# Performance work log

Hardware: AMD Instinct MI355X
Metric: run time of the kernel (lower is better)

The kernel has to match this reference:

```python
import jax, jax.numpy as jnp
import numpy as np
import math

H, KV, D, HID, WIN = 8, 4, 256, 2048, 1024  # heads, kv heads, head_dim, hidden, sliding window
B, S = 1, 2048

def _rms(x, scale):
    # Gemma3RMSNorm: hardcoded 1e-6 eps, (1+scale) gain
    var = jnp.mean(jnp.square(x), axis=-1, keepdims=True)
    return x * jax.lax.rsqrt(var + 1e-6) * (1.0 + scale)

def _rot_half(x):
    x1, x2 = jnp.split(x, 2, axis=-1)
    return jnp.concatenate((-x2, x1), axis=-1)

def setup_inputs() -> dict:
    key = jax.random.key(0)
    ks = jax.random.split(key, 8)
    x = jax.random.normal(ks[0], (B, S, HID), jnp.float32)
    attn_mask = jnp.ones((B, S), jnp.bool_)
    segment_pos = jnp.broadcast_to(jnp.arange(S, dtype=jnp.int32)[None], (B, S))
    # true RoPE tables, theta=1e6 (Gemma3 global layers)
    inv_freq = 1.0 / (1e6 ** (np.arange(0, D, 2, dtype=np.float32) / D))
    ang = np.arange(S, dtype=np.float32)[:, None] * inv_freq[None, :]  # [S, D/2]
    emb = np.concatenate([ang, ang], axis=-1)                          # [S, D]
    cos = jnp.asarray(np.cos(emb), jnp.float32)[None]                  # [1, S, D]
    sin = jnp.asarray(np.sin(emb), jnp.float32)[None]
    sd = 1.0 / math.sqrt(HID)
    wq = jax.random.normal(ks[1], (HID, H * D), jnp.float32) * sd
    wk = jax.random.normal(ks[2], (HID, KV * D), jnp.float32) * sd
    wv = jax.random.normal(ks[3], (HID, KV * D), jnp.float32) * sd
    wo = jax.random.normal(ks[4], (H * D, HID), jnp.float32) * (1.0 / math.sqrt(H * D))
    q_scale = jnp.zeros((D,), jnp.float32)  # zeros_init as in module
    k_scale = jnp.zeros((D,), jnp.float32)
    return dict(x=x, attn_mask=attn_mask, segment_pos=segment_pos, cos=cos, sin=sin,
                wq=wq, wk=wk, wv=wv, wo=wo, q_scale=q_scale, k_scale=k_scale)

def reference(x, attn_mask, segment_pos, cos, sin, wq, wk, wv, wo, q_scale, k_scale):
    b, s, _ = x.shape
    # projections -> [b, h, s, d]
    q = (x @ wq).reshape(b, s, H, D).transpose(0, 2, 1, 3)
    k = (x @ wk).reshape(b, s, KV, D).transpose(0, 2, 1, 3)
    v = (x @ wv).reshape(b, s, KV, D).transpose(0, 2, 1, 3)
    # per-head QK RMSNorm
    q = _rms(q, q_scale)
    k = _rms(k, k_scale)
    # RoPE (cos/sin broadcast over head axis, unsqueeze_dim=1)
    c, sn = cos[:, None], sin[:, None]
    q = q * c + _rot_half(q) * sn
    k = k * c + _rot_half(k) * sn
    # GQA: repeat-interleave kv heads
    rep = H // KV
    k = jnp.repeat(k, rep, axis=1)
    v = jnp.repeat(v, rep, axis=1)
    scores = jnp.einsum('bhqd,bhkd->bhqk', q, k) / math.sqrt(D)
    # causal + padding mask (q_len > 1 path, no image bidirectional mask)
    causal = jnp.tril(jnp.ones((s, s), jnp.bool_))
    mask = causal[None] & attn_mask[:, None, :]          # [b, q, kv]
    # sliding window mask (prefill: cache positions = arange)
    kvpos = jnp.arange(s)
    pos = segment_pos[:, :, None]
    sliding = (kvpos[None, None] > pos - WIN) & (kvpos[None, None] < pos + WIN)
    full = mask & sliding
    scores = scores + jnp.where(full[:, None], 0.0, -1e37)
    w = jax.nn.softmax(scores.astype(jnp.float32), axis=-1).astype(scores.dtype)
    out = jnp.einsum('bhqk,bhkd->bhqd', w, v)
    out = out.transpose(0, 2, 1, 3).reshape(b, s, H * D)
    return out @ wo
```

## Files before the change

kernel.cpp:

```cpp
#include <hip/hip_runtime.h>
#include <hip/hip_bf16.h>

#define S_LEN 2048
#define HID 2048
#define NH 8
#define NKV 4
#define HD 256
#define WIN 1024

typedef __hip_bfloat16 bf16;
typedef __attribute__((ext_vector_type(8))) short bf16x8;
typedef __attribute__((ext_vector_type(4))) float f32x4;

__device__ __forceinline__ void gld_lds16(void* lds, const void* g) {
    __builtin_amdgcn_global_load_lds(
        (const __attribute__((address_space(1))) unsigned int*)g,
        (__attribute__((address_space(3))) unsigned int*)lds,
        16, 0, 0);
}


__global__ __launch_bounds__(256)
void conv_f32_bf16(const float* __restrict__ s, bf16* __restrict__ d, int n8) {
    const int i = blockIdx.x * 256 + threadIdx.x;
    if (i >= n8) return;
    float4 a = ((const float4*)s)[i * 2];
    float4 b = ((const float4*)s)[i * 2 + 1];
    union { uint4 v; bf16 h[8]; } u;
    u.h[0] = __float2bfloat16(a.x); u.h[1] = __float2bfloat16(a.y);
    u.h[2] = __float2bfloat16(a.z); u.h[3] = __float2bfloat16(a.w);
    u.h[4] = __float2bfloat16(b.x); u.h[5] = __float2bfloat16(b.y);
    u.h[6] = __float2bfloat16(b.z); u.h[7] = __float2bfloat16(b.w);
    ((uint4*)d)[i] = u.v;
}

__device__ __forceinline__ void transT_body(const float* __restrict__ src, bf16* __restrict__ dst,
                                            int R, int C, int r0, int c0) {
    __shared__ bf16 Ts[64][72];
    const int tid = threadIdx.x;
    {
        const int r = tid >> 2;
        const int cq = (tid & 3) * 16;
#pragma unroll
        for (int j = 0; j < 16; j += 4) {
            float4 v = *(const float4*)&src[(size_t)(r0 + r) * C + c0 + cq + j];
            Ts[cq + j + 0][r] = __float2bfloat16(v.x);
            Ts[cq + j + 1][r] = __float2bfloat16(v.y);
            Ts[cq + j + 2][r] = __float2bfloat16(v.z);
            Ts[cq + j + 3][r] = __float2bfloat16(v.w);
        }
    }
    __syncthreads();
    {
        const int c = tid >> 2;
        const int rq = (tid & 3) * 16;
#pragma unroll
        for (int j = 0; j < 16; j += 8)
            *(uint4*)&dst[(size_t)(c0 + c) * R + r0 + rq + j] = *(const uint4*)&Ts[c][rq + j];
    }
}

__global__ __launch_bounds__(256)
void convT_f32_bf16(const float* __restrict__ src, bf16* __restrict__ dst, int R, int C) {
    transT_body(src, dst, R, C, blockIdx.y * 64, blockIdx.x * 64);
}

__global__ __launch_bounds__(256)
void convT_qkv(const float* __restrict__ wq, const float* __restrict__ wk,
               const float* __restrict__ wv, bf16* __restrict__ dst) {
    const int bx = blockIdx.x;
    const float* src; int C, c0, drow0;
    if (bx < 32)      { src = wq; C = 2048; c0 = bx * 64;        drow0 = bx * 64; }
    else if (bx < 48) { src = wk; C = 1024; c0 = (bx - 32) * 64; drow0 = 2048 + (bx - 32) * 64; }
    else              { src = wv; C = 1024; c0 = (bx - 48) * 64; drow0 = 3072 + (bx - 48) * 64; }
    bf16* dshift = dst + ((size_t)drow0 - c0) * HID;
    transT_body(src, dshift, HID, C, blockIdx.y * 64, c0);
}

template<int MODE>
__global__ __launch_bounds__(256)
void gemm_m97(const bf16* __restrict__ A, const bf16* __restrict__ Bt,
              float* __restrict__ C, bf16* __restrict__ Cb,
              bf16* __restrict__ Qo, bf16* __restrict__ Ko, bf16* __restrict__ Vto,
              int N, int K, int KS) {
    __shared__ bf16 As[128][32];
    __shared__ bf16 Bs[128][32];
    const int tid = threadIdx.x;
    const int w = tid >> 6, lane = tid & 63;
    const int lnm = lane & 15, quad = lane >> 4;
    const int wm = (w & 1) * 64, wn = (w >> 1) * 64;
    const int m0 = blockIdx.y * 128, n0 = blockIdx.x * 128;
    const int kbeg = (MODE == 2) ? blockIdx.z * KS : 0;
    const int kend = (MODE == 2) ? kbeg + KS : K;

    const int lr = lane >> 2;
    const int lc = (lane & 3) * 8;

    f32x4 acc[4][4];
#pragma unroll
    for (int i = 0; i < 4; ++i)
#pragma unroll
        for (int j = 0; j < 4; ++j) acc[i][j] = (f32x4){0.f, 0.f, 0.f, 0.f};

    const bf16* ga0 = A  + (size_t)(m0 + 32 * w + lr) * K + lc;
    const bf16* ga1 = ga0 + (size_t)16 * K;
    const bf16* gb0 = Bt + (size_t)(n0 + 32 * w + lr) * K + lc;
    const bf16* gb1 = gb0 + (size_t)16 * K;

    for (int k0 = kbeg; k0 < kend; k0 += 32) {
        gld_lds16(&As[32 * w][0],      ga0 + k0);
        gld_lds16(&As[32 * w + 16][0], ga1 + k0);
        gld_lds16(&Bs[32 * w][0],      gb0 + k0);
        gld_lds16(&Bs[32 * w + 16][0], gb1 + k0);
        __syncthreads();

        bf16x8 af[4], bfr[4];
#pragma unroll
        for (int t = 0; t < 4; ++t) {
            af[t]  = *(const bf16x8*)&As[wm + t * 16 + lnm][quad * 8];
            bfr[t] = *(const bf16x8*)&Bs[wn + t * 16 + lnm][quad * 8];
        }
#pragma unroll
        for (int tm = 0; tm < 4; ++tm)
#pragma unroll
            for (int tn = 0; tn < 4; ++tn)
                acc[tm][tn] = __builtin_amdgcn_mfma_f32_16x16x32_bf16(
                    af[tm], bfr[tn], acc[tm][tn], 0, 0, 0);
        __syncthreads();
    }

#pragma unroll
    for (int tm = 0; tm < 4; ++tm)
#pragma unroll
        for (int tn = 0; tn < 4; ++tn)
#pragma unroll
            for (int r = 0; r < 4; ++r) {
                const int row = m0 + wm + tm * 16 + quad * 4 + r;
                const int col = n0 + wn + tn * 16 + lnm;
                const float v = acc[tm][tn][r];
                if constexpr (MODE == 0) {
                    C[(size_t)row * N + col] = v;
                } else if constexpr (MODE == 2) {
                    Cb[(size_t)blockIdx.z * 2048 * 2048 + (size_t)row * N + col] =
                        __float2bfloat16(v);
                } else {
                    if (col < 2048)
                        Qo[(size_t)row * (NH * HD) + col] = __float2bfloat16(v);
                    else if (col < 3072)
                        Ko[(size_t)row * (NKV * HD) + col - 2048] = __float2bfloat16(v);
                    else
                        Vto[(size_t)(col - 3072) * S_LEN + row] = __float2bfloat16(v);
                }
            }
}

__global__ __launch_bounds__(256)
void splitk_add(const bf16* __restrict__ p, float* __restrict__ out) {
    const int i = blockIdx.x * 256 + threadIdx.x;
    union { uint4 v; bf16 h[8]; } a, b;
    a.v = ((const uint4*)p)[i];
    b.v = ((const uint4*)(p + (size_t)2048 * 2048))[i];
    float4 o0, o1;
    o0.x = (float)a.h[0] + (float)b.h[0]; o0.y = (float)a.h[1] + (float)b.h[1];
    o0.z = (float)a.h[2] + (float)b.h[2]; o0.w = (float)a.h[3] + (float)b.h[3];
    o1.x = (float)a.h[4] + (float)b.h[4]; o1.y = (float)a.h[5] + (float)b.h[5];
    o1.z = (float)a.h[6] + (float)b.h[6]; o1.w = (float)a.h[7] + (float)b.h[7];
    ((float4*)out)[i * 2]     = o0;
    ((float4*)out)[i * 2 + 1] = o1;
}

__global__ __launch_bounds__(64)
void rmsrope_kernel(bf16* __restrict__ Q, bf16* __restrict__ Kb,
                    const float* __restrict__ cosb, const float* __restrict__ sinb,
                    const float* __restrict__ qscale, const float* __restrict__ kscale,
                    float qmul) {
    const int p = blockIdx.x;
    const int hg = blockIdx.y;
    const int lane = threadIdx.x;

    bf16* base;
    const float* scale;
    float mul;
    if (hg < NH) { base = Q + (size_t)p * (NH * HD) + hg * HD; scale = qscale; mul = qmul; }
    else         { base = Kb + (size_t)p * (NKV * HD) + (hg - NH) * HD; scale = kscale; mul = 1.f; }

    const int d0 = lane * 2;
    float x0 = (float)base[d0],       x1 = (float)base[d0 + 1];
    float y0 = (float)base[d0 + 128], y1 = (float)base[d0 + 129];

    float ss = x0 * x0 + x1 * x1 + y0 * y0 + y1 * y1;
#pragma unroll
    for (int off = 32; off > 0; off >>= 1) ss += __shfl_xor(ss, off, 64);
    const float r = rsqrtf(ss * (1.0f / (float)HD) + 1e-6f);

    x0 *= r * (1.f + scale[d0]);
    x1 *= r * (1.f + scale[d0 + 1]);
    y0 *= r * (1.f + scale[d0 + 128]);
    y1 *= r * (1.f + scale[d0 + 129]);

    const size_t cb = (size_t)p * HD;
    const float c0 = cosb[cb + d0],       c1 = cosb[cb + d0 + 1];
    const float cA = cosb[cb + d0 + 128], cB = cosb[cb + d0 + 129];
    const float s0 = sinb[cb + d0],       s1 = sinb[cb + d0 + 1];
    const float sA = sinb[cb + d0 + 128], sB = sinb[cb + d0 + 129];

    base[d0]       = __float2bfloat16((x0 * c0 - y0 * s0) * mul);
    base[d0 + 1]   = __float2bfloat16((x1 * c1 - y1 * s1) * mul);
    base[d0 + 128] = __float2bfloat16((y0 * cA + x0 * sA) * mul);
    base[d0 + 129] = __float2bfloat16((y1 * cB + x1 * sB) * mul);
}

#define NCHUNK 4
__global__ __launch_bounds__(256)
void attn_mfma(const bf16* __restrict__ Q, const bf16* __restrict__ K,
               const bf16* __restrict__ Vt, bf16* __restrict__ Op,
               float2* __restrict__ ml) {
    __shared__ bf16 Ks[32][264];
    __shared__ bf16 Vs[256][40];
    __shared__ bf16 Pl[4][16][40];
    const int qt = blockIdx.x, h = blockIdx.y, chunk = blockIdx.z, kvh = h >> 1;
    const int tid = threadIdx.x, w = tid >> 6, lane = tid & 63;
    const int lnm = lane & 15, quad = lane >> 4;

    bf16x8 qf[8];
    const int qrow = qt * 64 + w * 16 + lnm;
#pragma unroll
    for (int s = 0; s < 8; ++s)
        qf[s] = *(const bf16x8*)&Q[(size_t)qrow * HID + h * HD + s * 32 + quad * 8];

    f32x4 o[16];
#pragma unroll
    for (int i = 0; i < 16; ++i) o[i] = (f32x4){0.f, 0.f, 0.f, 0.f};
    float M[4] = {-3e38f, -3e38f, -3e38f, -3e38f};
    float L[4] = {0.f, 0.f, 0.f, 0.f};

    const int ktlo = (qt >= 16) ? (2 * qt - 32) : 0;
    const int kthi = 2 * qt + 1;
    const int ntile = kthi - ktlo + 1;
    const int c0 = ktlo + (chunk * ntile) / NCHUNK;
    const int c1 = ktlo + ((chunk + 1) * ntile) / NCHUNK - 1;

    for (int kt = c0; kt <= c1; ++kt) {
#pragma unroll
        for (int p = 0; p < 4; ++p) {
            const int row = p * 8 + (tid >> 5);
            const int d8 = (tid & 31) * 8;
            *(uint4*)&Ks[row][d8] =
                *(const uint4*)&K[(size_t)(kt * 32 + row) * (NKV * HD) + kvh * HD + d8];
        }
#pragma unroll
        for (int p = 0; p < 4; ++p) {
            const int d = p * 64 + (tid >> 2);
            const int c8 = (tid & 3) * 8;
            *(uint4*)&Vs[d][c8] =
                *(const uint4*)&Vt[(size_t)(kvh * HD + d) * S_LEN + kt * 32 + c8];
        }
        __syncthreads();

        f32x4 s4[2];
        s4[0] = (f32x4){0.f, 0.f, 0.f, 0.f};
        s4[1] = (f32x4){0.f, 0.f, 0.f, 0.f};
#pragma unroll
        for (int t = 0; t < 2; ++t)
#pragma unroll
            for (int s = 0; s < 8; ++s) {
                bf16x8 kf = *(const bf16x8*)&Ks[t * 16 + lnm][s * 32 + quad * 8];
                s4[t] = __builtin_amdgcn_mfma_f32_16x16x32_bf16(qf[s], kf, s4[t], 0, 0, 0);
            }
#pragma unroll
        for (int t = 0; t < 2; ++t)
#pragma unroll
            for (int r = 0; r < 4; ++r) {
                const int m_g = qt * 64 + w * 16 + quad * 4 + r;
                const int n_g = kt * 32 + t * 16 + lnm;
                if (n_g > m_g || n_g + (WIN - 1) < m_g) s4[t][r] = -1e30f;
            }
        float mx[4], rs[4], al[4];
#pragma unroll
        for (int r = 0; r < 4; ++r) {
            mx[r] = fmaxf(s4[0][r], s4[1][r]);
#pragma unroll
            for (int off = 1; off < 16; off <<= 1)
                mx[r] = fmaxf(mx[r], __shfl_xor(mx[r], off, 64));
            const float Mn = fmaxf(M[r], mx[r]);
            al[r] = __expf(M[r] - Mn);
            M[r] = Mn;
        }
#pragma unroll
        for (int t = 0; t < 2; ++t)
#pragma unroll
            for (int r = 0; r < 4; ++r)
                s4[t][r] = __expf(s4[t][r] - M[r]);
#pragma unroll
        for (int r = 0; r < 4; ++r) {
            rs[r] = s4[0][r] + s4[1][r];
#pragma unroll
            for (int off = 1; off < 16; off <<= 1)
                rs[r] += __shfl_xor(rs[r], off, 64);
            L[r] = L[r] * al[r] + rs[r];
        }
#pragma unroll
        for (int t2 = 0; t2 < 16; ++t2)
#pragma unroll
            for (int r = 0; r < 4; ++r) o[t2][r] *= al[r];
#pragma unroll
        for (int t = 0; t < 2; ++t)
#pragma unroll
            for (int r = 0; r < 4; ++r)
                Pl[w][quad * 4 + r][t * 16 + lnm] = __float2bfloat16(s4[t][r]);
        bf16x8 pa = *(const bf16x8*)&Pl[w][lnm][quad * 8];
#pragma unroll
        for (int t2 = 0; t2 < 16; ++t2) {
            bf16x8 vb = *(const bf16x8*)&Vs[t2 * 16 + lnm][quad * 8];
            o[t2] = __builtin_amdgcn_mfma_f32_16x16x32_bf16(pa, vb, o[t2], 0, 0, 0);
        }
        __syncthreads();
    }

    float rL[4];
#pragma unroll
    for (int r = 0; r < 4; ++r) rL[r] = (L[r] > 0.f) ? (1.f / L[r]) : 0.f;
    bf16* Opc = Op + (size_t)chunk * S_LEN * HID;
#pragma unroll
    for (int t2 = 0; t2 < 16; ++t2)
#pragma unroll
        for (int r = 0; r < 4; ++r)
            Opc[(size_t)(qt * 64 + w * 16 + quad * 4 + r) * HID + h * HD + t2 * 16 + lnm] =
                __float2bfloat16(o[t2][r] * rL[r]);
    if (lnm == 0) {
#pragma unroll
        for (int r = 0; r < 4; ++r) {
            const int row = qt * 64 + w * 16 + quad * 4 + r;
            ml[((size_t)chunk * S_LEN + row) * NH + h] = make_float2(M[r], L[r]);
        }
    }
}

__global__ __launch_bounds__(256)
void attn_combine(const bf16* __restrict__ Op, const float2* __restrict__ ml,
                  bf16* __restrict__ O) {
    const int row = blockIdx.x, h = blockIdx.y, d = threadIdx.x;
    float2 c[NCHUNK];
    float Mx = -3e38f;
#pragma unroll
    for (int i = 0; i < NCHUNK; ++i) {
        c[i] = ml[((size_t)i * S_LEN + row) * NH + h];
        Mx = fmaxf(Mx, c[i].x);
    }
    float wsum = 0.f, wgt[NCHUNK];
#pragma unroll
    for (int i = 0; i < NCHUNK; ++i) {
        wgt[i] = c[i].y * __expf(c[i].x - Mx);
        wsum += wgt[i];
    }
    const float inv = 1.0f / wsum;
    const size_t idx = (size_t)row * HID + h * HD + d;
    float acc = 0.f;
#pragma unroll
    for (int i = 0; i < NCHUNK; ++i)
        acc += wgt[i] * (float)Op[(size_t)i * S_LEN * HID + idx];
    O[idx] = __float2bfloat16(acc * inv);
}

extern "C" void kernel_launch(void* const* d_in, const int* in_sizes, int n_in,
                              void* d_out, int out_size, void* d_ws, size_t ws_size,
                              hipStream_t stream) {
    const float* xf   = (const float*)d_in[0];
    const float* cosb = (const float*)d_in[3];
    const float* sinb = (const float*)d_in[4];
    const float* wqf  = (const float*)d_in[5];
    const float* wkf  = (const float*)d_in[6];
    const float* wvf  = (const float*)d_in[7];
    const float* wof  = (const float*)d_in[8];
    const float* qs   = (const float*)d_in[9];
    const float* ks   = (const float*)d_in[10];
    float* out = (float*)d_out;
    char* ws = (char*)d_ws;

    bf16*   wot   = (bf16*)(ws);
    bf16*   Qb    = (bf16*)(ws + ( 8ull << 20));
    bf16*   Kb    = (bf16*)(ws + (16ull << 20));
    bf16*   Vtb   = (bf16*)(ws + (20ull << 20));
    bf16*   wqkvt = (bf16*)(ws + (24ull << 20));
    bf16*   xb    = (bf16*)(ws + (40ull << 20));
    bf16*   Op    = (bf16*)(ws + (24ull << 20));
    bf16*   Ab    = (bf16*)(ws + (40ull << 20));
    bf16*   pk    = (bf16*)(ws + (24ull << 20));
    float2* ml    = (float2*)(ws + (56ull << 20));

    dim3 blk(256);

    conv_f32_bf16<<<2048, blk, 0, stream>>>(xf, xb, (S_LEN * HID) / 8);
    convT_qkv<<<dim3(64, 32), blk, 0, stream>>>(wqf, wkf, wvf, wqkvt);
    convT_f32_bf16<<<dim3(32, 32), blk, 0, stream>>>(wof, wot, NH * HD, HID);

    gemm_m97<1><<<dim3(32, 16), blk, 0, stream>>>(
        xb, wqkvt, nullptr, nullptr, Qb, Kb, Vtb, 4096, HID, 0);

    rmsrope_kernel<<<dim3(S_LEN, NH + NKV), dim3(64), 0, stream>>>(
        Qb, Kb, cosb, sinb, qs, ks, 0.0625f);

    attn_mfma<<<dim3(S_LEN / 64, NH, NCHUNK), blk, 0, stream>>>(Qb, Kb, Vtb, Op, ml);
    attn_combine<<<dim3(S_LEN, NH), blk, 0, stream>>>(Op, ml, Ab);

    gemm_m97<2><<<dim3(16, 16, 2), blk, 0, stream>>>(
        Ab, wot, nullptr, pk, nullptr, nullptr, nullptr, HID, HID, 1024);
    splitk_add<<<2048, blk, 0, stream>>>(pk, out);
}
```

Before: 303.6 us.

## Double-buffer GEMM LDS tiles and fuse the three conversion kernels into one launch

The GEMM now keeps two LDS stages and issues the global-to-LDS loads for the next K tile before computing on the current one. This drops one barrier per iteration and overlaps load latency with MFMA work. The x conversion and the two weight transpose/convert kernels are merged into a single prep_all launch indexed by block id, which removes two launch boundaries. Double buffering doubles LDS per block, which may cut occupancy.

New measurement: 295.1 us. 1.03x faster.

```diff
diff --git a/kernel.cpp b/kernel.cpp
--- a/kernel.cpp
+++ b/kernel.cpp
@@ -19,20 +19,6 @@
         16, 0, 0);
 }
 
-
-__global__ __launch_bounds__(256)
-void conv_f32_bf16(const float* __restrict__ s, bf16* __restrict__ d, int n8) {
-    const int i = blockIdx.x * 256 + threadIdx.x;
-    if (i >= n8) return;
-    float4 a = ((const float4*)s)[i * 2];
-    float4 b = ((const float4*)s)[i * 2 + 1];
-    union { uint4 v; bf16 h[8]; } u;
-    u.h[0] = __float2bfloat16(a.x); u.h[1] = __float2bfloat16(a.y);
-    u.h[2] = __float2bfloat16(a.z); u.h[3] = __float2bfloat16(a.w);
-    u.h[4] = __float2bfloat16(b.x); u.h[5] = __float2bfloat16(b.y);
-    u.h[6] = __float2bfloat16(b.z); u.h[7] = __float2bfloat16(b.w);
-    ((uint4*)d)[i] = u.v;
-}
 
 __device__ __forceinline__ void transT_body(const float* __restrict__ src, bf16* __restrict__ dst,
                                             int R, int C, int r0, int c0) {
@@ -61,37 +47,52 @@
 }
 
 __global__ __launch_bounds__(256)
-void convT_f32_bf16(const float* __restrict__ src, bf16* __restrict__ dst, int R, int C) {
-    transT_body(src, dst, R, C, blockIdx.y * 64, blockIdx.x * 64);
-}
-
-__global__ __launch_bounds__(256)
-void convT_qkv(const float* __restrict__ wq, const float* __restrict__ wk,
-               const float* __restrict__ wv, bf16* __restrict__ dst) {
-    const int bx = blockIdx.x;
-    const float* src; int C, c0, drow0;
-    if (bx < 32)      { src = wq; C = 2048; c0 = bx * 64;        drow0 = bx * 64; }
-    else if (bx < 48) { src = wk; C = 1024; c0 = (bx - 32) * 64; drow0 = 2048 + (bx - 32) * 64; }
-    else              { src = wv; C = 1024; c0 = (bx - 48) * 64; drow0 = 3072 + (bx - 48) * 64; }
-    bf16* dshift = dst + ((size_t)drow0 - c0) * HID;
-    transT_body(src, dshift, HID, C, blockIdx.y * 64, c0);
+void prep_all(const float* __restrict__ xf, const float* __restrict__ wqf,
+              const float* __restrict__ wkf, const float* __restrict__ wvf,
+              const float* __restrict__ wof,
+              bf16* __restrict__ xb, bf16* __restrict__ wqkvt, bf16* __restrict__ wot) {
+    const int bid = blockIdx.x;
+    if (bid < 2048) {
+        const int i = bid * 256 + threadIdx.x;
+        float4 a = ((const float4*)xf)[i * 2];
+        float4 b = ((const float4*)xf)[i * 2 + 1];
+        union { uint4 v; bf16 h[8]; } u;
+        u.h[0] = __float2bfloat16(a.x); u.h[1] = __float2bfloat16(a.y);
+        u.h[2] = __float2bfloat16(a.z); u.h[3] = __float2bfloat16(a.w);
+        u.h[4] = __float2bfloat16(b.x); u.h[5] = __float2bfloat16(b.y);
+        u.h[6] = __float2bfloat16(b.z); u.h[7] = __float2bfloat16(b.w);
+        ((uint4*)xb)[i] = u.v;
+    } else if (bid < 4096) {
+        const int t = bid - 2048;
+        const int bx = t & 63, by = t >> 6;
+        const float* src; int C, c0, drow0;
+        if (bx < 32)      { src = wqf; C = 2048; c0 = bx * 64;        drow0 = bx * 64; }
+        else if (bx < 48) { src = wkf; C = 1024; c0 = (bx - 32) * 64; drow0 = 2048 + (bx - 32) * 64; }
+        else              { src = wvf; C = 1024; c0 = (bx - 48) * 64; drow0 = 3072 + (bx - 48) * 64; }
+        bf16* dshift = wqkvt + ((size_t)drow0 - c0) * HID;
+        transT_body(src, dshift, HID, C, by * 64, c0);
+    } else {
+        const int t = bid - 4096;
+        const int bx = t & 31, by = t >> 5;
+        transT_body(wof, wot, NH * HD, HID, by * 64, bx * 64);
+    }
 }
 
 template<int MODE>
 __global__ __launch_bounds__(256)
-void gemm_m97(const bf16* __restrict__ A, const bf16* __restrict__ Bt,
-              float* __restrict__ C, bf16* __restrict__ Cb,
-              bf16* __restrict__ Qo, bf16* __restrict__ Ko, bf16* __restrict__ Vto,
-              int N, int K, int KS) {
-    __shared__ bf16 As[128][32];
-    __shared__ bf16 Bs[128][32];
+void gemm_m97d(const bf16* __restrict__ A, const bf16* __restrict__ Bt,
+               bf16* __restrict__ Cb,
+               bf16* __restrict__ Qo, bf16* __restrict__ Ko, bf16* __restrict__ Vto,
+               int N, int K, int KS) {
+    __shared__ bf16 As[2][128][32];
+    __shared__ bf16 Bs[2][128][32];
     const int tid = threadIdx.x;
     const int w = tid >> 6, lane = tid & 63;
     const int lnm = lane & 15, quad = lane >> 4;
     const int wm = (w & 1) * 64, wn = (w >> 1) * 64;
     const int m0 = blockIdx.y * 128, n0 = blockIdx.x * 128;
     const int kbeg = (MODE == 2) ? blockIdx.z * KS : 0;
-    const int kend = (MODE == 2) ? kbeg + KS : K;
+    const int nk = ((MODE == 2) ? KS : K) / 32;
 
     const int lr = lane >> 2;
     const int lc = (lane & 3) * 8;
@@ -102,23 +103,31 @@
 #pragma unroll
         for (int j = 0; j < 4; ++j) acc[i][j] = (f32x4){0.f, 0.f, 0.f, 0.f};
 
-    const bf16* ga0 = A  + (size_t)(m0 + 32 * w + lr) * K + lc;
+    const bf16* ga0 = A  + (size_t)(m0 + 32 * w + lr) * K + kbeg + lc;
     const bf16* ga1 = ga0 + (size_t)16 * K;
-    const bf16* gb0 = Bt + (size_t)(n0 + 32 * w + lr) * K + lc;
+    const bf16* gb0 = Bt + (size_t)(n0 + 32 * w + lr) * K + kbeg + lc;
     const bf16* gb1 = gb0 + (size_t)16 * K;
 
-    for (int k0 = kbeg; k0 < kend; k0 += 32) {
-        gld_lds16(&As[32 * w][0],      ga0 + k0);
-        gld_lds16(&As[32 * w + 16][0], ga1 + k0);
-        gld_lds16(&Bs[32 * w][0],      gb0 + k0);
-        gld_lds16(&Bs[32 * w + 16][0], gb1 + k0);
+    gld_lds16(&As[0][32 * w][0],      ga0);
+    gld_lds16(&As[0][32 * w + 16][0], ga1);
+    gld_lds16(&Bs[0][32 * w][0],      gb0);
+    gld_lds16(&Bs[0][32 * w + 16][0], gb1);
+
+    int cur = 0;
+    for (int i = 0; i < nk; ++i) {
         __syncthreads();
-
+        if (i + 1 < nk) {
+            const int ko = (i + 1) * 32;
+            gld_lds16(&As[cur ^ 1][32 * w][0],      ga0 + ko);
+            gld_lds16(&As[cur ^ 1][32 * w + 16][0], ga1 + ko);
+            gld_lds16(&Bs[cur ^ 1][32 * w][0],      gb0 + ko);
+            gld_lds16(&Bs[cur ^ 1][32 * w + 16][0], gb1 + ko);
+        }
         bf16x8 af[4], bfr[4];
 #pragma unroll
         for (int t = 0; t < 4; ++t) {
-            af[t]  = *(const bf16x8*)&As[wm + t * 16 + lnm][quad * 8];
-            bfr[t] = *(const bf16x8*)&Bs[wn + t * 16 + lnm][quad * 8];
+            af[t]  = *(const bf16x8*)&As[cur][wm + t * 16 + lnm][quad * 8];
+            bfr[t] = *(const bf16x8*)&Bs[cur][wn + t * 16 + lnm][quad * 8];
         }
 #pragma unroll
         for (int tm = 0; tm < 4; ++tm)
@@ -126,7 +135,7 @@
             for (int tn = 0; tn < 4; ++tn)
                 acc[tm][tn] = __builtin_amdgcn_mfma_f32_16x16x32_bf16(
                     af[tm], bfr[tn], acc[tm][tn], 0, 0, 0);
-        __syncthreads();
+        cur ^= 1;
     }
 
 #pragma unroll
@@ -138,9 +147,7 @@
                 const int row = m0 + wm + tm * 16 + quad * 4 + r;
                 const int col = n0 + wn + tn * 16 + lnm;
                 const float v = acc[tm][tn][r];
-                if constexpr (MODE == 0) {
-                    C[(size_t)row * N + col] = v;
-                } else if constexpr (MODE == 2) {
+                if constexpr (MODE == 2) {
                     Cb[(size_t)blockIdx.z * 2048 * 2048 + (size_t)row * N + col] =
                         __float2bfloat16(v);
                 } else {
@@ -390,12 +397,10 @@
 
     dim3 blk(256);
 
-    conv_f32_bf16<<<2048, blk, 0, stream>>>(xf, xb, (S_LEN * HID) / 8);
-    convT_qkv<<<dim3(64, 32), blk, 0, stream>>>(wqf, wkf, wvf, wqkvt);
-    convT_f32_bf16<<<dim3(32, 32), blk, 0, stream>>>(wof, wot, NH * HD, HID);
-
-    gemm_m97<1><<<dim3(32, 16), blk, 0, stream>>>(
-        xb, wqkvt, nullptr, nullptr, Qb, Kb, Vtb, 4096, HID, 0);
+    prep_all<<<5120, blk, 0, stream>>>(xf, wqf, wkf, wvf, wof, xb, wqkvt, wot);
+
+    gemm_m97d<1><<<dim3(32, 16), blk, 0, stream>>>(
+        xb, wqkvt, nullptr, Qb, Kb, Vtb, 4096, HID, 0);
 
     rmsrope_kernel<<<dim3(S_LEN, NH + NKV), dim3(64), 0, stream>>>(
         Qb, Kb, cosb, sinb, qs, ks, 0.0625f);
@@ -403,7 +408,7 @@
     attn_mfma<<<dim3(S_LEN / 64, NH, NCHUNK), blk, 0, stream>>>(Qb, Kb, Vtb, Op, ml);
     attn_combine<<<dim3(S_LEN, NH), blk, 0, stream>>>(Op, ml, Ab);
 
-    gemm_m97<2><<<dim3(16, 16, 2), blk, 0, stream>>>(
-        Ab, wot, nullptr, pk, nullptr, nullptr, nullptr, HID, HID, 1024);
+    gemm_m97d<2><<<dim3(16, 16, 2), blk, 0, stream>>>(
+        Ab, wot, pk, nullptr, nullptr, nullptr, HID, HID, 1024);
     splitk_add<<<2048, blk, 0, stream>>>(pk, out);
 }
```
